# Kernel tuning notes

Hardware: AMD Instinct MI355X
Metric: run time of the kernel (lower is better)

Reference implementation:

```python
import jax, jax.numpy as jnp
import numpy as np

N_DENSE = 13
N_SPARSE = 26
VOCAB = 100000
EMB_DIM = 64
ATTN_HIDDEN = 12
BATCH = 8192
TEMP = 0.1

# pair indices (i < j) over the 26 sparse fields -> 325 pairs
_ROW, _COL = np.triu_indices(N_SPARSE, k=1)


def setup_inputs() -> dict:
    key = jax.random.key(0)
    ks = jax.random.split(key, 10)
    return {
        "dense_x": jax.random.normal(ks[0], (BATCH, N_DENSE), dtype=jnp.float32),
        "sparse_idx": jax.random.randint(ks[1], (BATCH, N_SPARSE), 0, VOCAB, dtype=jnp.int32),
        "emb_tables": jax.random.normal(ks[2], (N_SPARSE, VOCAB, EMB_DIM), dtype=jnp.float32) * 0.01,
        "attn_W": jax.random.normal(ks[3], (EMB_DIM, ATTN_HIDDEN), dtype=jnp.float32) * 0.1,
        "attn_b": jnp.zeros((ATTN_HIDDEN,), dtype=jnp.float32),
        "proj_W": jax.random.normal(ks[4], (ATTN_HIDDEN, 1), dtype=jnp.float32) * 0.1,
        "proj_b": jnp.zeros((1,), dtype=jnp.float32),
        "lin_W": jax.random.normal(ks[5], (N_DENSE + N_SPARSE, 1), dtype=jnp.float32) * 0.01,
        "lin_b": jnp.zeros((1,), dtype=jnp.float32),
        "pred_W": jax.random.normal(ks[6], (EMB_DIM, 1), dtype=jnp.float32) * 0.1,
        "pred_b": jnp.zeros((1,), dtype=jnp.float32),
    }


def reference(dense_x, sparse_idx, emb_tables, attn_W, attn_b, proj_W, proj_b,
              lin_W, lin_b, pred_W, pred_b):
    # linear part operates on the raw concatenated input (sparse ids as floats,
    # exactly as the torch module does via linear_part(x))
    x = jnp.concatenate([dense_x, sparse_idx.astype(jnp.float32)], axis=1)  # [B, 39]
    part_1 = x @ lin_W + lin_b  # [B, 1]

    # per-field embedding gather: [B, 26, D]
    field_ids = jnp.arange(N_SPARSE)[None, :]
    emb = emb_tables[field_ids, sparse_idx]

    # pairwise element-wise cross products: [B, 325, D]
    cross = emb[:, _ROW, :] * emb[:, _COL, :]

    # attention MLP + softmax over pairs (temperature 0.1)
    h = jax.nn.relu(cross @ attn_W + attn_b)            # [B, 325, 12]
    logits = (h @ proj_W + proj_b) / TEMP               # [B, 325, 1]
    scores = jax.nn.softmax(logits, axis=1)

    att_out = jnp.sum(cross * scores, axis=1)           # [B, D]
    part_2 = att_out @ pred_W + pred_b                  # [B, 1]
    return jax.nn.sigmoid(part_1 + part_2)
```

## Files before the change

### kernel.cpp

```cpp
#include <hip/hip_runtime.h>
#include <math.h>

#define N_DENSE  13
#define N_SPARSE 26
#define VOCAB    100000
#define EMB      64
#define NH       12
#define NPAIR    325
#define NTILE    21
#define NPADH    336
#define EBROW    72
#define EBSLOT   1888
#define TEMP_INV 10.0f

typedef __attribute__((ext_vector_type(8))) _Float16 f16x8;
typedef __attribute__((ext_vector_type(4))) float    f32x4;

__device__ __forceinline__ int ebbase(int f) { return f * EBROW + (((f >> 3) & 3) << 3); }

__global__ __launch_bounds__(128, 5) void afm_kernel(
    const float* __restrict__ dense_x,
    const int*   __restrict__ sparse_idx,
    const float* __restrict__ emb,
    const float* __restrict__ attn_W,
    const float* __restrict__ attn_b,
    const float* __restrict__ proj_W,
    const float* __restrict__ proj_b,
    const float* __restrict__ lin_W,
    const float* __restrict__ lin_b,
    const float* __restrict__ pred_W,
    const float* __restrict__ pred_b,
    float* __restrict__ out)
{
    const int tid  = threadIdx.x;
    const int lane = tid & 63;
    const int wv   = tid >> 6;
    const int q    = lane >> 4;
    const int c16  = lane & 15;
    const int row  = __builtin_amdgcn_readfirstlane(blockIdx.x * 2 + wv);

    __shared__ __align__(16) unsigned short eb_s[2][EBSLOT];
    __shared__ __align__(16) unsigned short ptab_s[NPADH];

    unsigned short* ebw = &eb_s[wv][0];

    const int* sidx = sparse_idx + row * N_SPARSE;
    int myid = (lane < N_SPARSE) ? sidx[lane] : 0;

    float4 vg[7];
    #pragma unroll
    for (int k = 0; k < 7; ++k) {
        int q2  = lane + 64 * k;
        int q2c = q2 < N_SPARSE * 16 ? q2 : N_SPARSE * 16 - 1;
        int f = q2c >> 4, d4 = q2c & 15;
        int idk = __shfl(myid, f);
        vg[k] = *(reinterpret_cast<const float4*>(
                    emb + ((size_t)f * VOCAB + (size_t)idk) * EMB) + d4);
    }

    f16x8 wf[2];
    {
        #pragma unroll
        for (int kt = 0; kt < 2; ++kt) {
            union { f16x8 v; unsigned u32[4]; } u;
            #pragma unroll
            for (int jp = 0; jp < 4; ++jp) {
                int d0 = kt * 32 + q * 8 + jp * 2;
                float w0, w1;
                if (c16 < NH)       { w0 = attn_W[d0 * NH + c16];
                                      w1 = attn_W[(d0 + 1) * NH + c16]; }
                else if (c16 == NH) { w0 = pred_W[d0];
                                      w1 = pred_W[d0 + 1]; }
                else                { w0 = 0.f; w1 = 0.f; }
                auto hh = __builtin_amdgcn_cvt_pkrtz(w0, w1);
                __builtin_memcpy(&u.u32[jp], &hh, 4);
            }
            wf[kt] = u.v;
        }
    }
    float b4[4], pwh[4];
    #pragma unroll
    for (int r = 0; r < 4; ++r) {
        int h = q * 4 + r;
        bool ok = (h < NH);
        b4[r]  = ok ? attn_b[h] : 0.0f;
        pwh[r] = ok ? proj_W[h] : 0.0f;
    }
    const float pb = proj_b[0];

    #pragma unroll 1
    for (int p = lane; p < NPADH; p += 64) {
        int pc = p < NPAIR ? p : NPAIR - 1;
        float sf = sqrtf((float)(2601 - 8 * pc));
        int i = (int)((51.0f - sf) * 0.5f);
        int st = (i * (51 - i)) >> 1;
        if (pc < st) { --i; st = (i * (51 - i)) >> 1; }
        else { int st2 = ((i + 1) * (50 - i)) >> 1; if (pc >= st2) { ++i; st = st2; } }
        int j = i + 1 + (pc - st);
        ptab_s[p] = (unsigned short)(i | (j << 8));
    }

    int srcf = lane - N_DENSE;
    int idsh = __shfl(myid, (srcf >= 0 && srcf < N_SPARSE) ? srcf : 0);
    float p1t = 0.0f;
    if (lane < N_DENSE) {
        p1t = dense_x[row * N_DENSE + lane] * lin_W[lane];
    } else if (lane < N_DENSE + N_SPARSE) {
        p1t = (float)idsh * lin_W[lane];
    }

    #pragma unroll
    for (int k = 0; k < 7; ++k) {
        int q2 = lane + 64 * k;
        if (q2 < N_SPARSE * 16) {
            int f = q2 >> 4, d4 = q2 & 15;
            auto h01 = __builtin_amdgcn_cvt_pkrtz(vg[k].x, vg[k].y);
            auto h23 = __builtin_amdgcn_cvt_pkrtz(vg[k].z, vg[k].w);
            uint2 pk;
            __builtin_memcpy(&pk.x, &h01, 4);
            __builtin_memcpy(&pk.y, &h23, 4);
            *reinterpret_cast<uint2*>(&ebw[ebbase(f) + d4 * 4]) = pk;
        }
    }

    float lsum = 0.0f, vsum = 0.0f;
    #pragma unroll 3
    for (int t = 0; t < NTILE; ++t) {
        unsigned pt = ptab_s[t * 16 + c16];
        int i = pt & 0xff, j = pt >> 8;

        const f16x8* pi = reinterpret_cast<const f16x8*>(ebw + ebbase(i));
        const f16x8* pj = reinterpret_cast<const f16x8*>(ebw + ebbase(j));
        f16x8 ca = pi[q] * pj[q];
        f16x8 cb = pi[q + 4] * pj[q + 4];

        __builtin_amdgcn_s_setprio(1);
        f32x4 acc = {0.f, 0.f, 0.f, 0.f};
        acc = __builtin_amdgcn_mfma_f32_16x16x32_f16(wf[0], ca, acc, 0, 0, 0);
        acc = __builtin_amdgcn_mfma_f32_16x16x32_f16(wf[1], cb, acc, 0, 0, 0);
        __builtin_amdgcn_s_setprio(0);

        float par =       fmaxf(acc[0] + b4[0], 0.f) * pwh[0];
        par = fmaf(fmaxf(acc[1] + b4[1], 0.f), pwh[1], par);
        par = fmaf(fmaxf(acc[2] + b4[2], 0.f), pwh[2], par);
        par = fmaf(fmaxf(acc[3] + b4[3], 0.f), pwh[3], par);
        float m = (q == 3) ? acc[0] : 0.0f;

        par += __shfl_xor(par, 16);
        par += __shfl_xor(par, 32);
        m   += __shfl_xor(m, 16);
        m   += __shfl_xor(m, 32);

        float ev = __expf((par + pb) * TEMP_INV);
        ev = ((t * 16 + c16) < NPAIR) ? ev : 0.0f;
        lsum += ev;
        vsum = fmaf(ev, m, vsum);
    }

    float p1 = p1t;
    #pragma unroll
    for (int o = 32; o > 0; o >>= 1) {
        lsum += __shfl_xor(lsum, o);
        vsum += __shfl_xor(vsum, o);
        p1   += __shfl_xor(p1, o);
    }
    if (lane == 0) {
        float z = p1 + lin_b[0] + vsum / lsum + pred_b[0];
        out[row] = 1.0f / (1.0f + __expf(-z));
    }
}

extern "C" void kernel_launch(void* const* d_in, const int* in_sizes, int n_in,
                              void* d_out, int out_size, void* d_ws, size_t ws_size,
                              hipStream_t stream)
{
    const float* dense_x = (const float*)d_in[0];
    const int*   sparse  = (const int*)  d_in[1];
    const float* emb     = (const float*)d_in[2];
    const float* attn_W  = (const float*)d_in[3];
    const float* attn_b  = (const float*)d_in[4];
    const float* proj_W  = (const float*)d_in[5];
    const float* proj_b  = (const float*)d_in[6];
    const float* lin_W   = (const float*)d_in[7];
    const float* lin_b   = (const float*)d_in[8];
    const float* pred_W  = (const float*)d_in[9];
    const float* pred_b  = (const float*)d_in[10];
    float* out = (float*)d_out;

    int rows = in_sizes[0] / N_DENSE;
    afm_kernel<<<rows / 2, 128, 0, stream>>>(dense_x, sparse, emb, attn_W, attn_b,
                                             proj_W, proj_b, lin_W, lin_b,
                                             pred_W, pred_b, out);
}
```

Measured before the change: 34.35 us.

## Process two batch rows per wavefront and drop redundant mask shuffles

Each wavefront now gathers embeddings for two rows at once and interleaves their MFMA and softmax work. This amortises the weight-fragment setup and pair-table lookups, and gives more independent memory loads and MFMAs in flight per wave. The cross-lane reduction of the MFMA output used as the attended value is removed and compensated with a factor of 4 in the final division. The cost is higher register pressure: 13 float4 gathers per lane, a launch bound lowered to 4 blocks, and half as many blocks, which may reduce latency hiding for the gather-bound phase.

```diff
diff --git a/kernel.cpp b/kernel.cpp
--- a/kernel.cpp
+++ b/kernel.cpp
@@ -18,7 +18,7 @@
 
 __device__ __forceinline__ int ebbase(int f) { return f * EBROW + (((f >> 3) & 3) << 3); }
 
-__global__ __launch_bounds__(128, 5) void afm_kernel(
+__global__ __launch_bounds__(128, 4) void afm_kernel(
     const float* __restrict__ dense_x,
     const int*   __restrict__ sparse_idx,
     const float* __restrict__ emb,
@@ -37,23 +37,26 @@
     const int wv   = tid >> 6;
     const int q    = lane >> 4;
     const int c16  = lane & 15;
-    const int row  = __builtin_amdgcn_readfirstlane(blockIdx.x * 2 + wv);
-
-    __shared__ __align__(16) unsigned short eb_s[2][EBSLOT];
+    const int row0 = __builtin_amdgcn_readfirstlane(blockIdx.x * 4 + wv * 2);
+
+    __shared__ __align__(16) unsigned short eb_s[2][2][EBSLOT];
     __shared__ __align__(16) unsigned short ptab_s[NPADH];
 
-    unsigned short* ebw = &eb_s[wv][0];
-
-    const int* sidx = sparse_idx + row * N_SPARSE;
-    int myid = (lane < N_SPARSE) ? sidx[lane] : 0;
-
-    float4 vg[7];
-    #pragma unroll
-    for (int k = 0; k < 7; ++k) {
-        int q2  = lane + 64 * k;
-        int q2c = q2 < N_SPARSE * 16 ? q2 : N_SPARSE * 16 - 1;
-        int f = q2c >> 4, d4 = q2c & 15;
-        int idk = __shfl(myid, f);
+    unsigned short* ebw0 = &eb_s[wv][0][0];
+    unsigned short* ebw1 = &eb_s[wv][1][0];
+
+    int l32 = lane & 31;
+    int myid = (l32 < N_SPARSE)
+             ? sparse_idx[(row0 + (lane >> 5)) * N_SPARSE + l32] : 0;
+
+    float4 vg[13];
+    #pragma unroll
+    for (int k = 0; k < 13; ++k) {
+        int q2   = lane + 64 * k;
+        int rsel = q2 >= 416;
+        int loc  = q2 - (rsel ? 416 : 0);
+        int f = loc >> 4, d4 = loc & 15;
+        int idk = __shfl(myid, (rsel << 5) + f);
         vg[k] = *(reinterpret_cast<const float4*>(
                     emb + ((size_t)f * VOCAB + (size_t)idk) * EMB) + d4);
     }
@@ -100,73 +103,98 @@
         ptab_s[p] = (unsigned short)(i | (j << 8));
     }
 
-    int srcf = lane - N_DENSE;
-    int idsh = __shfl(myid, (srcf >= 0 && srcf < N_SPARSE) ? srcf : 0);
-    float p1t = 0.0f;
+    int srcf  = lane - N_DENSE;
+    bool idok = (srcf >= 0 && srcf < N_SPARSE);
+    int id0 = __shfl(myid, idok ? srcf : 0);
+    int id1 = __shfl(myid, 32 + (idok ? srcf : 0));
+    float p1t0 = 0.0f, p1t1 = 0.0f;
     if (lane < N_DENSE) {
-        p1t = dense_x[row * N_DENSE + lane] * lin_W[lane];
+        p1t0 = dense_x[row0 * N_DENSE + lane] * lin_W[lane];
+        p1t1 = dense_x[(row0 + 1) * N_DENSE + lane] * lin_W[lane];
     } else if (lane < N_DENSE + N_SPARSE) {
-        p1t = (float)idsh * lin_W[lane];
-    }
-
-    #pragma unroll
-    for (int k = 0; k < 7; ++k) {
-        int q2 = lane + 64 * k;
-        if (q2 < N_SPARSE * 16) {
-            int f = q2 >> 4, d4 = q2 & 15;
-            auto h01 = __builtin_amdgcn_cvt_pkrtz(vg[k].x, vg[k].y);
-            auto h23 = __builtin_amdgcn_cvt_pkrtz(vg[k].z, vg[k].w);
-            uint2 pk;
-            __builtin_memcpy(&pk.x, &h01, 4);
-            __builtin_memcpy(&pk.y, &h23, 4);
-            *reinterpret_cast<uint2*>(&ebw[ebbase(f) + d4 * 4]) = pk;
-        }
-    }
-
-    float lsum = 0.0f, vsum = 0.0f;
-    #pragma unroll 3
+        p1t0 = (float)id0 * lin_W[lane];
+        p1t1 = (float)id1 * lin_W[lane];
+    }
+
+    #pragma unroll
+    for (int k = 0; k < 13; ++k) {
+        int q2   = lane + 64 * k;
+        int rsel = q2 >= 416;
+        int loc  = q2 - (rsel ? 416 : 0);
+        int f = loc >> 4, d4 = loc & 15;
+        auto h01 = __builtin_amdgcn_cvt_pkrtz(vg[k].x, vg[k].y);
+        auto h23 = __builtin_amdgcn_cvt_pkrtz(vg[k].z, vg[k].w);
+        uint2 pk;
+        __builtin_memcpy(&pk.x, &h01, 4);
+        __builtin_memcpy(&pk.y, &h23, 4);
+        unsigned short* dst = rsel ? ebw1 : ebw0;
+        *reinterpret_cast<uint2*>(&dst[ebbase(f) + d4 * 4]) = pk;
+    }
+
+    float lsum0 = 0.0f, vsum0 = 0.0f, lsum1 = 0.0f, vsum1 = 0.0f;
+    #pragma unroll 2
     for (int t = 0; t < NTILE; ++t) {
         unsigned pt = ptab_s[t * 16 + c16];
         int i = pt & 0xff, j = pt >> 8;
-
-        const f16x8* pi = reinterpret_cast<const f16x8*>(ebw + ebbase(i));
-        const f16x8* pj = reinterpret_cast<const f16x8*>(ebw + ebbase(j));
-        f16x8 ca = pi[q] * pj[q];
-        f16x8 cb = pi[q + 4] * pj[q + 4];
+        const int bi = ebbase(i), bj = ebbase(j);
+        const bool pv = (t * 16 + c16) < NPAIR;
+
+        const f16x8* pi0 = reinterpret_cast<const f16x8*>(ebw0 + bi);
+        const f16x8* pj0 = reinterpret_cast<const f16x8*>(ebw0 + bj);
+        const f16x8* pi1 = reinterpret_cast<const f16x8*>(ebw1 + bi);
+        const f16x8* pj1 = reinterpret_cast<const f16x8*>(ebw1 + bj);
+        f16x8 ca0 = pi0[q] * pj0[q], cb0 = pi0[q + 4] * pj0[q + 4];
+        f16x8 ca1 = pi1[q] * pj1[q], cb1 = pi1[q + 4] * pj1[q + 4];
 
         __builtin_amdgcn_s_setprio(1);
-        f32x4 acc = {0.f, 0.f, 0.f, 0.f};
-        acc = __builtin_amdgcn_mfma_f32_16x16x32_f16(wf[0], ca, acc, 0, 0, 0);
-        acc = __builtin_amdgcn_mfma_f32_16x16x32_f16(wf[1], cb, acc, 0, 0, 0);
+        f32x4 acc0 = {0.f, 0.f, 0.f, 0.f};
+        f32x4 acc1 = {0.f, 0.f, 0.f, 0.f};
+        acc0 = __builtin_amdgcn_mfma_f32_16x16x32_f16(wf[0], ca0, acc0, 0, 0, 0);
+        acc1 = __builtin_amdgcn_mfma_f32_16x16x32_f16(wf[0], ca1, acc1, 0, 0, 0);
+        acc0 = __builtin_amdgcn_mfma_f32_16x16x32_f16(wf[1], cb0, acc0, 0, 0, 0);
+        acc1 = __builtin_amdgcn_mfma_f32_16x16x32_f16(wf[1], cb1, acc1, 0, 0, 0);
         __builtin_amdgcn_s_setprio(0);
 
-        float par =       fmaxf(acc[0] + b4[0], 0.f) * pwh[0];
-        par = fmaf(fmaxf(acc[1] + b4[1], 0.f), pwh[1], par);
-        par = fmaf(fmaxf(acc[2] + b4[2], 0.f), pwh[2], par);
-        par = fmaf(fmaxf(acc[3] + b4[3], 0.f), pwh[3], par);
-        float m = (q == 3) ? acc[0] : 0.0f;
-
-        par += __shfl_xor(par, 16);
-        par += __shfl_xor(par, 32);
-        m   += __shfl_xor(m, 16);
-        m   += __shfl_xor(m, 32);
-
-        float ev = __expf((par + pb) * TEMP_INV);
-        ev = ((t * 16 + c16) < NPAIR) ? ev : 0.0f;
-        lsum += ev;
-        vsum = fmaf(ev, m, vsum);
-    }
-
-    float p1 = p1t;
+        float par0 =       fmaxf(acc0[0] + b4[0], 0.f) * pwh[0];
+        par0 = fmaf(fmaxf(acc0[1] + b4[1], 0.f), pwh[1], par0);
+        par0 = fmaf(fmaxf(acc0[2] + b4[2], 0.f), pwh[2], par0);
+        par0 = fmaf(fmaxf(acc0[3] + b4[3], 0.f), pwh[3], par0);
+        float par1 =       fmaxf(acc1[0] + b4[0], 0.f) * pwh[0];
+        par1 = fmaf(fmaxf(acc1[1] + b4[1], 0.f), pwh[1], par1);
+        par1 = fmaf(fmaxf(acc1[2] + b4[2], 0.f), pwh[2], par1);
+        par1 = fmaf(fmaxf(acc1[3] + b4[3], 0.f), pwh[3], par1);
+
+        par0 += __shfl_xor(par0, 16);
+        par1 += __shfl_xor(par1, 16);
+        par0 += __shfl_xor(par0, 32);
+        par1 += __shfl_xor(par1, 32);
+
+        float ev0 = __expf((par0 + pb) * TEMP_INV);
+        float ev1 = __expf((par1 + pb) * TEMP_INV);
+        ev0 = pv ? ev0 : 0.0f;
+        ev1 = pv ? ev1 : 0.0f;
+        lsum0 += ev0;
+        lsum1 += ev1;
+        float m0 = (q == 3) ? acc0[0] : 0.0f;
+        float m1 = (q == 3) ? acc1[0] : 0.0f;
+        vsum0 = fmaf(ev0, m0, vsum0);
+        vsum1 = fmaf(ev1, m1, vsum1);
+    }
+
     #pragma unroll
     for (int o = 32; o > 0; o >>= 1) {
-        lsum += __shfl_xor(lsum, o);
-        vsum += __shfl_xor(vsum, o);
-        p1   += __shfl_xor(p1, o);
+        lsum0 += __shfl_xor(lsum0, o);
+        vsum0 += __shfl_xor(vsum0, o);
+        lsum1 += __shfl_xor(lsum1, o);
+        vsum1 += __shfl_xor(vsum1, o);
+        p1t0  += __shfl_xor(p1t0, o);
+        p1t1  += __shfl_xor(p1t1, o);
     }
     if (lane == 0) {
-        float z = p1 + lin_b[0] + vsum / lsum + pred_b[0];
-        out[row] = 1.0f / (1.0f + __expf(-z));
+        float z0 = p1t0 + lin_b[0] + 4.0f * vsum0 / lsum0 + pred_b[0];
+        float z1 = p1t1 + lin_b[0] + 4.0f * vsum1 / lsum1 + pred_b[0];
+        out[row0]     = 1.0f / (1.0f + __expf(-z0));
+        out[row0 + 1] = 1.0f / (1.0f + __expf(-z1));
     }
 }
 
@@ -188,7 +216,7 @@
     float* out = (float*)d_out;
 
     int rows = in_sizes[0] / N_DENSE;
-    afm_kernel<<<rows / 2, 128, 0, stream>>>(dense_x, sparse, emb, attn_W, attn_b,
+    afm_kernel<<<rows / 4, 128, 0, stream>>>(dense_x, sparse, emb, attn_W, attn_b,
                                              proj_W, proj_b, lin_W, lin_b,
                                              pred_W, pred_b, out);
 }
```

Result: faster. 30.17 us, median of 2 (-12.2%).
